# Kernel tuning notes

Measured on AMD Instinct MI355X. Metric: run time of the kernel, lower is better.

## Reference

```python
import jax, jax.numpy as jnp
import numpy as np

DIM = 768
NUM_HEADS = 12
HEAD_DIM = DIM // NUM_HEADS
B, N = 16, 784


def setup_inputs() -> dict:
    key = jax.random.key(0)
    k1, k2, k3, k4, k5 = jax.random.split(key, 5)
    x = jax.random.normal(k1, (B, N, DIM), dtype=jnp.float32)
    # Dense params (flax Dense: kernel [in, out], bias [out])
    Wqkv = jax.random.normal(k2, (DIM, 3 * DIM), dtype=jnp.float32) * (DIM ** -0.5)
    bqkv = jnp.zeros((3 * DIM,), dtype=jnp.float32)
    Wo = jax.random.normal(k3, (DIM, DIM), dtype=jnp.float32) * (DIM ** -0.5)
    bo = jnp.zeros((DIM,), dtype=jnp.float32)
    return {"x": x, "Wqkv": Wqkv, "bqkv": bqkv, "Wo": Wo, "bo": bo}


def reference(x, Wqkv, bqkv, Wo, bo):
    b, n, dim = x.shape
    # fused QKV projection
    qkv = jnp.einsum('bnd,df->bnf', x, Wqkv) + bqkv          # [b, n, 3*dim]
    qkv = qkv.reshape(b, n, 3, NUM_HEADS, HEAD_DIM)           # '(k h d)' split
    q, k, v = qkv[:, :, 0], qkv[:, :, 1], qkv[:, :, 2]        # [b, n, h, d]
    scale = HEAD_DIM ** -0.5
    # chunked/flash path computes exact softmax attention; same math, expressed densely
    scores = jnp.einsum('bihd,bjhd->bhij', q, k) * scale      # [b, h, n, n]
    attn = jax.nn.softmax(scores, axis=-1)
    out = jnp.einsum('bhij,bjhd->bihd', attn, v)              # [b, n, h, d]
    out = out.reshape(b, n, dim)                              # 'b n (h d)'
    return jnp.einsum('bnd,df->bnf', out, Wo) + bo
```

## Files before the change

kernel.cpp:

```cpp
#include <hip/hip_runtime.h>

#define DIM 768
#define NHEADS 12
#define HDIM 64
#define BB 16
#define NN 784
#define M_TOTAL (BB * NN)

typedef __attribute__((ext_vector_type(8))) _Float16 f16x8;
typedef __attribute__((ext_vector_type(4))) float f32x4;
typedef __attribute__((ext_vector_type(16))) float f32x16;
typedef __fp16 fp16x2 __attribute__((ext_vector_type(2)));

typedef __attribute__((address_space(3))) unsigned int lds_uint;
typedef __attribute__((address_space(1))) const unsigned int g_uint;
__device__ inline void gload_lds16(const void* g, void* l) {
    __builtin_amdgcn_global_load_lds((g_uint*)(uintptr_t)g,
                                     (lds_uint*)(uintptr_t)l, 16, 0, 0);
}

#if __has_builtin(__builtin_amdgcn_exp2f)
#define EXP2(x) __builtin_amdgcn_exp2f(x)
#else
#define EXP2(x) exp2f(x)
#endif

__device__ inline unsigned int pk2(float a, float b, float* lacc) {
#if __has_builtin(__builtin_amdgcn_cvt_pkrtz)
    union { fp16x2 h; unsigned int u; } r;
    r.h = __builtin_amdgcn_cvt_pkrtz(a, b);
#if __has_builtin(__builtin_amdgcn_fdot2)
    const fp16x2 one = {(__fp16)1.f, (__fp16)1.f};
    *lacc = __builtin_amdgcn_fdot2(r.h, one, *lacc, false);
#else
    *lacc += a + b;
#endif
    return r.u;
#else
    union { _Float16 h[2]; unsigned int u; } r;
    r.h[0] = (_Float16)a; r.h[1] = (_Float16)b;
    *lacc += a + b;
    return r.u;
#endif
}

__global__ __launch_bounds__(256) void prep_kernel(
    const float* __restrict__ x, _Float16* __restrict__ xh,
    const float* __restrict__ Wqkv, _Float16* __restrict__ wqT,
    const float* __restrict__ Wo, _Float16* __restrict__ woT)
{
    const int NC  = (M_TOTAL * DIM) / (8 * 256);
    const int NQX = (3 * DIM) / 32;
    const int NQ  = NQX * (DIM / 32);
    const int NOX = DIM / 32;
    const int bid = blockIdx.x;

    if (bid < NC) {
        const int i = (bid * 256 + threadIdx.x) * 8;
        float4 a = *(const float4*)&x[i];
        float4 b = *(const float4*)&x[i + 4];
        union { _Float16 h[8]; uint4 v; } o;
        o.h[0] = (_Float16)a.x; o.h[1] = (_Float16)a.y;
        o.h[2] = (_Float16)a.z; o.h[3] = (_Float16)a.w;
        o.h[4] = (_Float16)b.x; o.h[5] = (_Float16)b.y;
        o.h[6] = (_Float16)b.z; o.h[7] = (_Float16)b.w;
        *(uint4*)&xh[i] = o.v;
        return;
    }

    __shared__ float t[32][33];
    const float* W; _Float16* T; int N, n0, k0;
    if (bid < NC + NQ) {
        const int lb = bid - NC;
        W = Wqkv; T = wqT; N = 3 * DIM;
        n0 = (lb % NQX) * 32; k0 = (lb / NQX) * 32;
    } else {
        const int lb = bid - NC - NQ;
        W = Wo; T = woT; N = DIM;
        n0 = (lb % NOX) * 32; k0 = (lb / NOX) * 32;
    }
    const int K = DIM;
    const int r = threadIdx.x >> 3, c4 = (threadIdx.x & 7) * 4;
    float4 v = *(const float4*)&W[(size_t)(k0 + r) * N + n0 + c4];
    t[r][c4 + 0] = v.x; t[r][c4 + 1] = v.y;
    t[r][c4 + 2] = v.z; t[r][c4 + 3] = v.w;
    __syncthreads();
    union { _Float16 h[4]; ushort4 v4; } o;
#pragma unroll
    for (int i = 0; i < 4; ++i) o.h[i] = (_Float16)t[c4 + i][r];
    *(ushort4*)&T[(size_t)(n0 + r) * K + k0 + c4] = o.v4;
}

#define VMCNT(N) asm volatile("s_waitcnt vmcnt(" #N ")" ::: "memory")
#define BARRIER() { asm volatile("" ::: "memory"); \
                    __builtin_amdgcn_s_barrier();  \
                    asm volatile("" ::: "memory"); }

#define ISSUE_A(BUF, K0, I)                                                    \
    gload_lds16(A + (size_t)(gm + (I) * 64 + w * 8 + srow) * K + (K0) + scol,  \
                &sA[BUF][((I) * 64 + w * 8) * 64]);
#define ISSUE_B(BUF, K0, I)                                                    \
    gload_lds16(B + (size_t)(gn + (I) * 64 + w * 8 + srow) * K + (K0) + scol,  \
                &sB[BUF][((I) * 64 + w * 8) * 64]);

#define READ_B()                                                               \
  { _Pragma("unroll")                                                          \
    for (int kk = 0; kk < 4; ++kk) {                                           \
        const int sw = ((kk * 2 + hi) ^ (l31 & 7)) * 8;                        \
        breg[0][kk] = *(const f16x8*)&sB[cur][(wn + l31) * 64 + sw];           \
        breg[1][kk] = *(const f16x8*)&sB[cur][(wn + 32 + l31) * 64 + sw];      \
    } }

#define READ_A(P)                                                              \
  { _Pragma("unroll")                                                          \
    for (int kk = 0; kk < 4; ++kk) {                                           \
        const int sw = ((kk * 2 + hi) ^ (l31 & 7)) * 8;                        \
        af[kk] = *(const f16x8*)&sA[cur][(wm + (P) * 32 + l31) * 64 + sw];     \
    } }

#define MFMA_P(P)                                                              \
  { __builtin_amdgcn_s_setprio(1);                                             \
    _Pragma("unroll")                                                          \
    for (int kk = 0; kk < 4; ++kk) {                                           \
        acc[P][0] = __builtin_amdgcn_mfma_f32_32x32x16_f16(                    \
            af[kk], breg[0][kk], acc[P][0], 0, 0, 0);                          \
        acc[P][1] = __builtin_amdgcn_mfma_f32_32x32x16_f16(                    \
            af[kk], breg[1][kk], acc[P][1], 0, 0, 0);                          \
    }                                                                          \
    __builtin_amdgcn_s_setprio(0); }

template <int OUT_F16>
__global__ __launch_bounds__(512) void gemm_f16_kernel(
    const _Float16* __restrict__ A, const _Float16* __restrict__ B,
    const float* __restrict__ bias, void* __restrict__ Cout,
    int M, int N, int K)
{
    __shared__ _Float16 sA[2][256 * 64];
    __shared__ _Float16 sB[2][256 * 64];

    const int tid  = threadIdx.x;
    const int w    = tid >> 6;
    const int lane = tid & 63;

    const int nwg = gridDim.x * gridDim.y;
    const int lid = blockIdx.x + gridDim.x * blockIdx.y;
    const int cq  = nwg >> 3, cr = nwg & 7;
    const int xcd = lid & 7, ix = lid >> 3;
    const int wgid = (xcd < cr ? xcd * (cq + 1) : cr * (cq + 1) + (xcd - cr) * cq) + ix;
    const int gn = (wgid % gridDim.x) * 256;
    const int gm = (wgid / gridDim.x) * 256;

    const int wm = (w & 1) * 128;
    const int wn = (w >> 1) * 64;
    const int l31 = lane & 31;
    const int hi  = lane >> 5;

    const int srow = lane >> 3;
    const int scol = ((lane & 7) ^ srow) * 8;

    f32x16 acc[4][2] = {};
    f16x8 breg[2][4], af[4];

    const int NT = K >> 6;

    ISSUE_B(0, 0, 0) ISSUE_B(0, 0, 1) ISSUE_B(0, 0, 2) ISSUE_B(0, 0, 3)
    ISSUE_A(0, 0, 0) ISSUE_A(0, 0, 2) ISSUE_A(0, 0, 1) ISSUE_A(0, 0, 3)
    VMCNT(2);
    BARRIER();

    int cur = 0;
#pragma unroll 1
    for (int t = 0; t < NT; ++t) {
        const int kn = (t + 1) * 64;
        const int nb = cur ^ 1;
        const bool more = (t + 1 < NT);
        if (more) { ISSUE_B(nb, kn, 0) ISSUE_B(nb, kn, 1) }
        READ_B()
        READ_A(0)
        MFMA_P(0)
        if (more) { ISSUE_B(nb, kn, 2) ISSUE_B(nb, kn, 3) }
        READ_A(1)
        MFMA_P(1)
        if (more) { VMCNT(4); } else { VMCNT(0); }
        BARRIER();
        if (more) { ISSUE_A(nb, kn, 0) ISSUE_A(nb, kn, 2) }
        READ_A(2)
        MFMA_P(2)
        if (more) { ISSUE_A(nb, kn, 1) ISSUE_A(nb, kn, 3) }
        READ_A(3)
        MFMA_P(3)
        if (more) { VMCNT(2); BARRIER(); }
        cur ^= 1;
    }

#pragma unroll
    for (int nt = 0; nt < 2; ++nt) {
        const int col = gn + wn + nt * 32 + l31;
        const float bv = bias[col];
#pragma unroll
        for (int mt = 0; mt < 4; ++mt) {
            f32x16 v = acc[mt][nt];
#pragma unroll
            for (int reg = 0; reg < 16; ++reg) {
                const int row = gm + wm + mt * 32 + (reg & 3) + 8 * (reg >> 2) + 4 * hi;
                const float o = v[reg] + bv;
                if (OUT_F16)
                    ((_Float16*)Cout)[(size_t)row * N + col] = (_Float16)o;
                else
                    ((float*)Cout)[(size_t)row * N + col] = o;
            }
        }
    }
}

#define LOG2E_8 0.18033688f

#define LOAD_TILE(J0, TAIL)                                                    \
  {                                                                            \
    const int j0_ = (J0);                                                      \
    int jrowK = j0_ + sj;                                                      \
    if (TAIL && jrowK > NN - 1) jrowK = NN - 1;                                \
    const size_t kbase = (size_t)(b * NN + jrowK) * (3 * DIM) + DIM + h * HDIM;\
    k0v = *(const uint4*)&qkv[kbase + sg * 8];                                 \
    k1v = *(const uint4*)&qkv[kbase + sg * 8 + 32];                            \
    int vr0 = j0_ + 2 * jj, vr1 = j0_ + 2 * jj + 1;                            \
    if (TAIL) { if (vr0 > NN - 1) vr0 = NN - 1; if (vr1 > NN - 1) vr1 = NN - 1; } \
    va.v = *(const uint4*)&qkv[(size_t)(b * NN + vr0) * (3 * DIM) + 2 * DIM + h * HDIM + dsub]; \
    vc.v = *(const uint4*)&qkv[(size_t)(b * NN + vr1) * (3 * DIM) + 2 * DIM + h * HDIM + dsub]; \
  }

#define WRITE_TILE(BUF)                                                        \
  {                                                                            \
    _Float16 (*K_)[72] = Ks[BUF];                                              \
    _Float16 (*V_)[72] = Vt[BUF];                                              \
    *(uint4*)&K_[sj][sg * 8]      = k0v;                                       \
    *(uint4*)&K_[sj][sg * 8 + 32] = k1v;                                       \
    _Pragma("unroll")                                                          \
    for (int i = 0; i < 8; ++i) {                                              \
        union { _Float16 h2[2]; unsigned int u; } t;                           \
        t.h2[0] = va.h[i]; t.h2[1] = vc.h[i];                                  \
        *(unsigned int*)&V_[dsub + i][pcol] = t.u;                             \
    }                                                                          \
  }

#define EXP_PACK(SV, G, J0_, TAIL)                                             \
  {                                                                            \
    float p0 = EXP2(SV[0]), p1 = EXP2(SV[1]);                                  \
    float p2 = EXP2(SV[2]), p3 = EXP2(SV[3]);                                  \
    if (TAIL && (J0_ + nt * 16) >= NN) { p0 = p1 = p2 = p3 = 0.f; }            \
    pk[G][nt][0] = pk2(p0, p1, &lpart[G]);                                     \
    pk[G][nt][1] = pk2(p2, p3, &lpart[G]);                                     \
  }

#define COMPUTE_TILE(BUF, J0, TAIL)                                            \
  {                                                                            \
    _Float16 (*K_)[72] = Ks[BUF];                                              \
    _Float16 (*V_)[72] = Vt[BUF];                                              \
    unsigned int pk[2][4][2];                                                  \
    _Pragma("unroll")                                                          \
    for (int nt = 0; nt < 4; ++nt) {                                           \
        f16x8 kf0 = *(const f16x8*)&K_[nt * 16 + l16][quad * 8];               \
        f16x8 kf1 = *(const f16x8*)&K_[nt * 16 + l16][32 + quad * 8];          \
        f32x4 s0 = {}, s1 = {};                                                \
        s0 = __builtin_amdgcn_mfma_f32_16x16x32_f16(kf0, qfrag[0][0], s0, 0, 0, 0); \
        s0 = __builtin_amdgcn_mfma_f32_16x16x32_f16(kf1, qfrag[0][1], s0, 0, 0, 0); \
        s1 = __builtin_amdgcn_mfma_f32_16x16x32_f16(kf0, qfrag[1][0], s1, 0, 0, 0); \
        s1 = __builtin_amdgcn_mfma_f32_16x16x32_f16(kf1, qfrag[1][1], s1, 0, 0, 0); \
        EXP_PACK(s0, 0, J0, TAIL)                                              \
        EXP_PACK(s1, 1, J0, TAIL)                                              \
    }                                                                          \
    __builtin_amdgcn_s_setprio(1);                                             \
    _Pragma("unroll")                                                          \
    for (int pc = 0; pc < 2; ++pc) {                                           \
        union { unsigned int u[4]; f16x8 v; } pa0, pa1;                        \
        pa0.u[0] = pk[0][2 * pc][0];     pa0.u[1] = pk[0][2 * pc][1];          \
        pa0.u[2] = pk[0][2 * pc + 1][0]; pa0.u[3] = pk[0][2 * pc + 1][1];      \
        pa1.u[0] = pk[1][2 * pc][0];     pa1.u[1] = pk[1][2 * pc][1];          \
        pa1.u[2] = pk[1][2 * pc + 1][0]; pa1.u[3] = pk[1][2 * pc + 1][1];      \
        _Pragma("unroll")                                                      \
        for (int dt = 0; dt < 4; ++dt) {                                       \
            f16x8 vf = *(const f16x8*)&V_[dt * 16 + l16][pc * 32 + quad * 8];  \
            O[0][dt] = __builtin_amdgcn_mfma_f32_16x16x32_f16(pa0.v, vf, O[0][dt], 0, 0, 0); \
            O[1][dt] = __builtin_amdgcn_mfma_f32_16x16x32_f16(pa1.v, vf, O[1][dt], 0, 0, 0); \
        }                                                                      \
    }                                                                          \
    __builtin_amdgcn_s_setprio(0);                                             \
  }

__global__ __launch_bounds__(256, 2) void attn_f16_kernel(
    const _Float16* __restrict__ qkv, _Float16* __restrict__ oat)
{
    const int L   = blockIdx.x + 7 * (blockIdx.y + NHEADS * blockIdx.z);
    const int xcd = L & 7, ixc = L >> 3;
    const int grp = xcd * 24 + ixc / 7;
    const int q0  = (ixc % 7) * 128;
    const int b   = grp / NHEADS;
    const int h   = grp % NHEADS;

    const int tid = threadIdx.x;
    const int wave = tid >> 6;
    const int lane = tid & 63;
    const int quad = lane >> 4;
    const int l16  = lane & 15;

    __shared__ _Float16 Ks[2][64][72];
    __shared__ _Float16 Vt[2][64][72];

    f16x8 qfrag[2][2];
#pragma unroll
    for (int g = 0; g < 2; ++g) {
        int qrow = q0 + wave * 32 + g * 16 + l16; if (qrow > NN - 1) qrow = NN - 1;
        size_t base = (size_t)(b * NN + qrow) * (3 * DIM) + h * HDIM;
        qfrag[g][0] = (*(const f16x8*)&qkv[base + quad * 8]) * (_Float16)LOG2E_8;
        qfrag[g][1] = (*(const f16x8*)&qkv[base + 32 + quad * 8]) * (_Float16)LOG2E_8;
    }

    const int sj = lane;
    const int sg = wave;
    const int jj   = lane & 31;
    const int dsub = sg * 16 + (lane >> 5) * 8;
    const int pcol = ((jj >> 4) << 5) | (((jj >> 1) & 3) << 3)
                   | (((jj >> 3) & 1) << 2) | ((jj & 1) << 1);

    f32x4 O[2][4] = {};
    float lpart[2] = {0.f, 0.f};

    uint4 k0v, k1v;
    union { uint4 v; _Float16 h[8]; } va, vc;

    LOAD_TILE(0, 0)
#pragma unroll 1
    for (int jt = 0; jt < 11; ++jt) {
        WRITE_TILE(jt & 1)
        __syncthreads();
        LOAD_TILE((jt + 1) * 64, 0)
        COMPUTE_TILE(jt & 1, 0, 0)
    }
    WRITE_TILE(1)
    __syncthreads();
    LOAD_TILE(768, 1)
    COMPUTE_TILE(1, 704, 0)
    WRITE_TILE(0)
    __syncthreads();
    COMPUTE_TILE(0, 768, 1)

#pragma unroll
    for (int g = 0; g < 2; ++g) {
        float t = lpart[g];
        t += __shfl_xor(t, 16);
        t += __shfl_xor(t, 32);
        float inv[4];
#pragma unroll
        for (int r = 0; r < 4; ++r)
            inv[r] = 1.0f / __shfl(t, quad * 4 + r, 16);
#pragma unroll
        for (int r = 0; r < 4; ++r) {
            const int q = q0 + wave * 32 + g * 16 + quad * 4 + r;
            if (q < NN) {
#pragma unroll
                for (int dt = 0; dt < 4; ++dt) {
                    const size_t base = (size_t)(b * NN + q) * DIM + h * HDIM + dt * 16 + l16;
                    oat[base] = (_Float16)(O[g][dt][r] * inv[r]);
                }
            }
        }
    }
}

extern "C" void kernel_launch(void* const* d_in, const int* in_sizes, int n_in,
                              void* d_out, int out_size, void* d_ws, size_t ws_size,
                              hipStream_t stream) {
    const float* x    = (const float*)d_in[0];
    const float* Wqkv = (const float*)d_in[1];
    const float* bqkv = (const float*)d_in[2];
    const float* Wo   = (const float*)d_in[3];
    const float* bo   = (const float*)d_in[4];
    float* out = (float*)d_out;

    _Float16* qkv = (_Float16*)d_ws;
    _Float16* xh  = qkv + (size_t)M_TOTAL * 3 * DIM;
    _Float16* wqT = xh + (size_t)M_TOTAL * DIM;
    _Float16* woT = wqT + (size_t)3 * DIM * DIM;
    _Float16* oat = xh;

    {
        const int NC = (M_TOTAL * DIM) / (8 * 256);
        const int NQ = ((3 * DIM) / 32) * (DIM / 32);
        const int NO_ = (DIM / 32) * (DIM / 32);
        prep_kernel<<<NC + NQ + NO_, 256, 0, stream>>>(
            x, xh, Wqkv, wqT, Wo, woT);
    }
    gemm_f16_kernel<1><<<dim3((3 * DIM) / 256, M_TOTAL / 256), 512, 0, stream>>>(
        xh, wqT, bqkv, qkv, M_TOTAL, 3 * DIM, DIM);
    attn_f16_kernel<<<dim3(7, NHEADS, BB), 256, 0, stream>>>(qkv, oat);
    gemm_f16_kernel<0><<<dim3(DIM / 256, M_TOTAL / 256), 512, 0, stream>>>(
        oat, woT, bo, out, M_TOTAL, DIM, DIM);
}
```

Baseline: 226.0 us.

## Use simpler double-buffered GEMM kernel for the QKV projection

Adds a new GEMM kernel that stages each 64-wide K slice of A and B into LDS with direct global-to-LDS loads. It double-buffers with one __syncthreads per iteration and computes a 4x2 set of 32x32 MFMA tiles per wave. The QKV projection now uses this kernel, while the output projection keeps the original finely pipelined kernel under a new name. The simpler schedule may cut instruction and wait overhead, but it may hide memory latency less well than the hand-tuned vmcnt-based pipeline.

```diff
diff --git a/kernel.cpp b/kernel.cpp
--- a/kernel.cpp
+++ b/kernel.cpp
@@ -91,6 +91,106 @@
     *(ushort4*)&T[(size_t)(n0 + r) * K + k0 + c4] = o.v4;
 }
 
+#define G_STAGE(BUF, K0)                                                       \
+  {                                                                            \
+    _Pragma("unroll")                                                          \
+    for (int i = 0; i < 4; ++i) {                                              \
+        const int rbase = w * 32 + i * 8;                                      \
+        gload_lds16(A + (size_t)(gm + rbase + srow) * K + (K0) + scol,         \
+                    &sA[BUF][rbase * 64]);                                     \
+        gload_lds16(B + (size_t)(gn + rbase + srow) * K + (K0) + scol,         \
+                    &sB[BUF][rbase * 64]);                                     \
+    }                                                                          \
+  }
+
+#define G_COMPUTE(BUF)                                                         \
+  {                                                                            \
+    _Pragma("unroll")                                                          \
+    for (int kk = 0; kk < 4; ++kk) {                                           \
+        const int c = kk * 2 + hi;                                             \
+        const int sw = (c ^ (l31 & 7)) * 8;                                    \
+        f16x8 a[4], bb[2];                                                     \
+        _Pragma("unroll")                                                      \
+        for (int mt = 0; mt < 4; ++mt)                                         \
+            a[mt] = *(const f16x8*)&sA[BUF][(wm + mt * 32 + l31) * 64 + sw];   \
+        _Pragma("unroll")                                                      \
+        for (int nt = 0; nt < 2; ++nt)                                         \
+            bb[nt] = *(const f16x8*)&sB[BUF][(wn + nt * 32 + l31) * 64 + sw];  \
+        __builtin_amdgcn_s_setprio(1);                                         \
+        _Pragma("unroll")                                                      \
+        for (int mt = 0; mt < 4; ++mt)                                         \
+            _Pragma("unroll")                                                  \
+            for (int nt = 0; nt < 2; ++nt)                                     \
+                acc[mt][nt] = __builtin_amdgcn_mfma_f32_32x32x16_f16(          \
+                    a[mt], bb[nt], acc[mt][nt], 0, 0, 0);                      \
+        __builtin_amdgcn_s_setprio(0);                                         \
+    }                                                                          \
+  }
+
+template <int OUT_F16>
+__global__ __launch_bounds__(512) void gemm_dbuf_kernel(
+    const _Float16* __restrict__ A, const _Float16* __restrict__ B,
+    const float* __restrict__ bias, void* __restrict__ Cout,
+    int M, int N, int K)
+{
+    __shared__ _Float16 sA[2][256 * 64];
+    __shared__ _Float16 sB[2][256 * 64];
+
+    const int tid  = threadIdx.x;
+    const int w    = tid >> 6;
+    const int lane = tid & 63;
+
+    const int nwg = gridDim.x * gridDim.y;
+    const int lid = blockIdx.x + gridDim.x * blockIdx.y;
+    const int cq  = nwg >> 3, cr = nwg & 7;
+    const int xcd = lid & 7, ix = lid >> 3;
+    const int wgid = (xcd < cr ? xcd * (cq + 1) : cr * (cq + 1) + (xcd - cr) * cq) + ix;
+    const int gn = (wgid % gridDim.x) * 256;
+    const int gm = (wgid / gridDim.x) * 256;
+
+    const int wm = (w & 1) * 128;
+    const int wn = (w >> 1) * 64;
+    const int l31 = lane & 31;
+    const int hi  = lane >> 5;
+
+    const int srow = lane >> 3;
+    const int scol = ((lane & 7) ^ srow) * 8;
+
+    f32x16 acc[4][2] = {};
+
+    const int NT = K >> 6;
+    G_STAGE(0, 0)
+    __syncthreads();
+    int cur = 0;
+#pragma unroll 1
+    for (int t = 0; t < NT - 1; ++t) {
+        G_STAGE(cur ^ 1, (t + 1) * 64)
+        G_COMPUTE(cur)
+        __syncthreads();
+        cur ^= 1;
+    }
+    G_COMPUTE(cur)
+
+#pragma unroll
+    for (int nt = 0; nt < 2; ++nt) {
+        const int col = gn + wn + nt * 32 + l31;
+        const float bv = bias[col];
+#pragma unroll
+        for (int mt = 0; mt < 4; ++mt) {
+            f32x16 v = acc[mt][nt];
+#pragma unroll
+            for (int reg = 0; reg < 16; ++reg) {
+                const int row = gm + wm + mt * 32 + (reg & 3) + 8 * (reg >> 2) + 4 * hi;
+                const float o = v[reg] + bv;
+                if (OUT_F16)
+                    ((_Float16*)Cout)[(size_t)row * N + col] = (_Float16)o;
+                else
+                    ((float*)Cout)[(size_t)row * N + col] = o;
+            }
+        }
+    }
+}
+
 #define VMCNT(N) asm volatile("s_waitcnt vmcnt(" #N ")" ::: "memory")
 #define BARRIER() { asm volatile("" ::: "memory"); \
                     __builtin_amdgcn_s_barrier();  \
@@ -130,7 +230,7 @@
     __builtin_amdgcn_s_setprio(0); }
 
 template <int OUT_F16>
-__global__ __launch_bounds__(512) void gemm_f16_kernel(
+__global__ __launch_bounds__(512) void gemm_quad_kernel(
     const _Float16* __restrict__ A, const _Float16* __restrict__ B,
     const float* __restrict__ bias, void* __restrict__ Cout,
     int M, int N, int K)
@@ -390,9 +490,9 @@
         prep_kernel<<<NC + NQ + NO_, 256, 0, stream>>>(
             x, xh, Wqkv, wqT, Wo, woT);
     }
-    gemm_f16_kernel<1><<<dim3((3 * DIM) / 256, M_TOTAL / 256), 512, 0, stream>>>(
+    gemm_dbuf_kernel<1><<<dim3((3 * DIM) / 256, M_TOTAL / 256), 512, 0, stream>>>(
         xh, wqT, bqkv, qkv, M_TOTAL, 3 * DIM, DIM);
     attn_f16_kernel<<<dim3(7, NHEADS, BB), 256, 0, stream>>>(qkv, oat);
-    gemm_f16_kernel<0><<<dim3(DIM / 256, M_TOTAL / 256), 512, 0, stream>>>(
+    gemm_quad_kernel<0><<<dim3(DIM / 256, M_TOTAL / 256), 512, 0, stream>>>(
         oat, woT, bo, out, M_TOTAL, DIM, DIM);
 }
```

After: 227.2 us. Within noise of the previous version (+0.5%).
